# Performance work log

Hardware: AMD Instinct MI355X
Metric: run time of the kernel (lower is better)

The kernel has to match this reference:

```python
import jax, jax.numpy as jnp
import numpy as np

IN_DIM = 1024
INNER_DIM = 4096
HEADS = 16
HEAD_DIM = 64
EPS = 1e-5


def layer_norm(x, gamma, beta):
    mu = jnp.mean(x, axis=-1, keepdims=True)
    var = jnp.mean(jnp.square(x - mu), axis=-1, keepdims=True)
    return (x - mu) * jax.lax.rsqrt(var + EPS) * gamma + beta


def setup_inputs() -> dict:
    key = jax.random.key(0)
    ks = jax.random.split(key, 12)
    B, N = 2, 2048
    s_in = 1.0 / np.sqrt(IN_DIM)
    s_inner = 1.0 / np.sqrt(INNER_DIM)
    return {
        "x": jax.random.normal(ks[0], (B, N, IN_DIM), jnp.float32),
        "w_qkv": jax.random.normal(ks[1], (IN_DIM, HEADS * HEAD_DIM * 3), jnp.float32) * s_in,
        "b_qkv": jnp.zeros((HEADS * HEAD_DIM * 3,), jnp.float32),
        "w_proj": jax.random.normal(ks[2], (HEADS * HEAD_DIM, IN_DIM), jnp.float32) * s_in,
        "b_proj": jnp.zeros((IN_DIM,), jnp.float32),
        "g1": jnp.ones((IN_DIM,), jnp.float32),
        "beta1": jnp.zeros((IN_DIM,), jnp.float32),
        "w_ff1": jax.random.normal(ks[3], (IN_DIM, INNER_DIM), jnp.float32) * s_in,
        "b_ff1": jnp.zeros((INNER_DIM,), jnp.float32),
        "w_ff2": jax.random.normal(ks[4], (INNER_DIM, IN_DIM), jnp.float32) * s_inner,
        "b_ff2": jnp.zeros((IN_DIM,), jnp.float32),
        "g2": jnp.ones((IN_DIM,), jnp.float32),
        "beta2": jnp.zeros((IN_DIM,), jnp.float32),
    }


def reference(x, w_qkv, b_qkv, w_proj, b_proj, g1, beta1, w_ff1, b_ff1, w_ff2, b_ff2, g2, beta2):
    B, N, _ = x.shape
    scale = HEAD_DIM ** -0.5
    # QKV projection: (B,N,H,3D) -> (B,H,N,3D), then split as in torch chunk
    qkv = (x @ w_qkv + b_qkv).reshape(B, N, HEADS, 3 * HEAD_DIM).transpose(0, 2, 1, 3)
    q, k, v = jnp.split(qkv, 3, axis=-1)  # each (B,H,N,D)
    attn = jax.nn.softmax(jnp.einsum("bhnd,bhmd->bhnm", q, k) * scale, axis=-1)
    out = jnp.einsum("bhnm,bhmd->bhnd", attn, v).transpose(0, 2, 1, 3).reshape(B, N, HEADS * HEAD_DIM)
    out = out @ w_proj + b_proj
    # residual + LN1
    h = layer_norm(out + x, g1, beta1)
    # FFN + residual + LN2
    ff = jax.nn.relu(h @ w_ff1 + b_ff1) @ w_ff2 + b_ff2
    return layer_norm(ff + h, g2, beta2)
```

## Files before the change

kernel.cpp:

```cpp
#include <hip/hip_runtime.h>

typedef unsigned short u16;
typedef unsigned int u32;
typedef __attribute__((ext_vector_type(8))) short short8;
typedef __attribute__((ext_vector_type(4))) float float4v;

#define MB (1024 * 1024)
#define AS1 __attribute__((address_space(1)))
#define AS3 __attribute__((address_space(3)))

__device__ inline float b2f(u16 u) {
    union { u32 i; float f; } v; v.i = ((u32)u) << 16; return v.f;
}
__device__ inline u16 f2b(float f) {
    union { float f; u32 i; } v; v.f = f;
    u32 r = (v.i + 0x7FFF + ((v.i >> 16) & 1)) >> 16;
    return (u16)r;
}
__device__ inline u32 pk2(float a, float b) { return (u32)f2b(a) | ((u32)f2b(b) << 16); }
__device__ inline u32 pk2t(float a, float b) {
    return __builtin_amdgcn_perm(__float_as_uint(b), __float_as_uint(a), 0x07060302u);
}

__global__ __launch_bounds__(256) void detect_dtype(const u16* __restrict__ x, u32* __restrict__ flag) {
    __shared__ int cnt;
    if (threadIdx.x == 0) cnt = 0;
    __syncthreads();
    int hits = 0;
    for (int i = threadIdx.x; i < 512; i += 256) {
        u16 w = x[2 * i];
        int e = (w >> 7) & 0xFF;
        if (e >= 116 && e <= 134) hits++;
    }
    atomicAdd(&cnt, hits);
    __syncthreads();
    if (threadIdx.x == 0) *flag = (cnt < 256) ? 1u : 0u;
}

__global__ __launch_bounds__(256) void convert_x(const void* __restrict__ src, u16* __restrict__ dst,
                                                 int n, const u32* __restrict__ flagp) {
    int i = (blockIdx.x * 256 + threadIdx.x) * 8;
    if (i >= n) return;
    if (*flagp) {
        const float* s = (const float*)src;
        float4 f0 = *(const float4*)(s + i);
        float4 f1 = *(const float4*)(s + i + 4);
        union { uint4 v; u16 u[8]; } O;
        O.u[0] = f2b(f0.x); O.u[1] = f2b(f0.y); O.u[2] = f2b(f0.z); O.u[3] = f2b(f0.w);
        O.u[4] = f2b(f1.x); O.u[5] = f2b(f1.y); O.u[6] = f2b(f1.z); O.u[7] = f2b(f1.w);
        *(uint4*)(dst + i) = O.v;
    } else {
        *(uint4*)(dst + i) = *(const uint4*)((const u16*)src + i);
    }
}

__global__ __launch_bounds__(256) void transpose_any(const void* __restrict__ src, u16* __restrict__ dst,
                                                     int ldS, int ldD, const u32* __restrict__ flagp) {
    __shared__ alignas(16) u16 tile[64 * 78];
    int c0 = blockIdx.x * 64, r0 = blockIdx.y * 64;
    int tid = threadIdx.x;
    u32 flg = *flagp;
#pragma unroll
    for (int it = 0; it < 2; ++it) {
        int idx = tid + it * 256;
        int rr = idx >> 3, cc = idx & 7;
        union { uint4 v; u16 u[8]; } U;
        if (flg) {
            const float* s = (const float*)src + (size_t)(r0 + rr) * ldS + c0 + cc * 8;
            float4 f0 = *(const float4*)(s);
            float4 f1 = *(const float4*)(s + 4);
            U.u[0] = f2b(f0.x); U.u[1] = f2b(f0.y); U.u[2] = f2b(f0.z); U.u[3] = f2b(f0.w);
            U.u[4] = f2b(f1.x); U.u[5] = f2b(f1.y); U.u[6] = f2b(f1.z); U.u[7] = f2b(f1.w);
        } else {
            U.v = *(const uint4*)((const u16*)src + (size_t)(r0 + rr) * ldS + c0 + cc * 8);
        }
#pragma unroll
        for (int j = 0; j < 8; ++j) tile[(cc * 8 + j) * 78 + rr] = U.u[j];
    }
    __syncthreads();
#pragma unroll
    for (int it = 0; it < 2; ++it) {
        int idx = tid + it * 256;
        int rr = idx >> 3, cc = idx & 7;
        const u32* t32 = (const u32*)(tile + rr * 78);
        uint4 v;
        v.x = t32[cc * 4 + 0]; v.y = t32[cc * 4 + 1]; v.z = t32[cc * 4 + 2]; v.w = t32[cc * 4 + 3];
        *(uint4*)(dst + (size_t)(c0 + rr) * ldD + r0 + cc * 8) = v;
    }
}

__global__ __launch_bounds__(256) void v_transpose(const u16* __restrict__ qkv, u16* __restrict__ vt) {
    __shared__ alignas(16) u16 tile[64 * 78];
    int n0 = blockIdx.x * 64;
    int bh = blockIdx.y, b = bh >> 4, h = bh & 15;
    const u16* src = qkv + (size_t)b * 2048 * 3072 + h * 192 + 128;
    int tid = threadIdx.x;
#pragma unroll
    for (int it = 0; it < 2; ++it) {
        int idx = tid + it * 256;
        int rr = idx >> 3, cc = idx & 7;
        union { uint4 v; u16 u[8]; } U;
        U.v = *(const uint4*)(src + (size_t)(n0 + rr) * 3072 + cc * 8);
#pragma unroll
        for (int j = 0; j < 8; ++j) tile[(cc * 8 + j) * 78 + rr] = U.u[j];
    }
    __syncthreads();
#pragma unroll
    for (int it = 0; it < 2; ++it) {
        int idx = tid + it * 256;
        int rr = idx >> 3, cc = idx & 7;
        const u32* t32 = (const u32*)(tile + rr * 78);
        uint4 v;
        v.x = t32[cc * 4 + 0]; v.y = t32[cc * 4 + 1]; v.z = t32[cc * 4 + 2]; v.w = t32[cc * 4 + 3];
        *(uint4*)(vt + ((size_t)bh * 64 + rr) * 2048 + n0 + cc * 8) = v;
    }
}

template <int BN>
__global__ __launch_bounds__(256) void gemm_bt(const u16* __restrict__ A, const u16* __restrict__ Bt,
                                               const void* __restrict__ bias, u16* __restrict__ Cb,
                                               float* __restrict__ Cf,
                                               int M, int N, int K, int relu,
                                               const u32* __restrict__ flagp) {
    __shared__ alignas(16) u16 sA[128 * 32];
    __shared__ alignas(16) u16 sB[BN * 32];
    constexpr int WMT = (BN == 128) ? 4 : 2;
    int tid = threadIdx.x;
    int n0 = blockIdx.x * BN, m0 = blockIdx.y * 128;
    int wave = tid >> 6, lane = tid & 63, l15 = lane & 15, quad = lane >> 4;
    int wm = (BN == 128) ? (wave >> 1) * 64 : wave * 32;
    int wn = (BN == 128) ? (wave & 1) * 64 : 0;
    float4v acc[WMT][4] = {};

    for (int k0 = 0; k0 < K; k0 += 32) {
        __syncthreads();
#pragma unroll
        for (int it = 0; it < 2; ++it) {
            int idx = it * 256 + tid;
            int rr = idx >> 2, kc = idx & 3;
            __builtin_amdgcn_global_load_lds(
                (const AS1 void*)(A + (size_t)(m0 + rr) * K + k0 + kc * 8),
                (AS3 void*)&sA[(it * 256 + wave * 64) * 8], 16, 0, 0);
        }
#pragma unroll
        for (int it = 0; it < BN / 64; ++it) {
            int idx = it * 256 + tid;
            int rr = idx >> 2, kc = idx & 3;
            __builtin_amdgcn_global_load_lds(
                (const AS1 void*)(Bt + (size_t)(n0 + rr) * K + k0 + kc * 8),
                (AS3 void*)&sB[(it * 256 + wave * 64) * 8], 16, 0, 0);
        }
        __syncthreads();
        short8 a[WMT], b[4];
#pragma unroll
        for (int mi = 0; mi < WMT; ++mi) a[mi] = *(const short8*)&sA[(wm + mi * 16 + l15) * 32 + quad * 8];
#pragma unroll
        for (int ni = 0; ni < 4; ++ni) b[ni] = *(const short8*)&sB[(wn + ni * 16 + l15) * 32 + quad * 8];
#pragma unroll
        for (int mi = 0; mi < WMT; ++mi)
#pragma unroll
            for (int ni = 0; ni < 4; ++ni)
                acc[mi][ni] = __builtin_amdgcn_mfma_f32_16x16x32_bf16(a[mi], b[ni], acc[mi][ni], 0, 0, 0);
    }
    u32 flg = *flagp;
#pragma unroll
    for (int ni = 0; ni < 4; ++ni) {
        int col = n0 + wn + ni * 16 + l15;
        float bv = flg ? ((const float*)bias)[col] : b2f(((const u16*)bias)[col]);
#pragma unroll
        for (int mi = 0; mi < WMT; ++mi) {
#pragma unroll
            for (int r = 0; r < 4; ++r) {
                int row = m0 + wm + mi * 16 + quad * 4 + r;
                float v = acc[mi][ni][r] + bv;
                if (relu) v = fmaxf(v, 0.f);
                if (Cf) Cf[(size_t)row * N + col] = v;
                else    Cb[(size_t)row * N + col] = f2b(v);
            }
        }
    }
}

__global__ __launch_bounds__(256) void attn_kernel(const u16* __restrict__ qkv, const u16* __restrict__ vt,
                                                   u16* __restrict__ outp) {
    __shared__ alignas(16) u16 sK[2][64 * 64];
    __shared__ alignas(16) u16 sV[2][64 * 64];
    __shared__ alignas(16) u16 sP[4][32 * 68];
    const float C2 = 0.18033688011112042f;
    const float MT = -17.312340490667560f;
    int tid = threadIdx.x;
    int wave = tid >> 6, lane = tid & 63, l15 = lane & 15, quad = lane >> 4;
    int bh = blockIdx.x, b = bh >> 4, h = bh & 15;
    int m0 = blockIdx.y * 128 + wave * 32;
    const size_t hq = (size_t)b * 2048 * 3072 + (size_t)h * 192;
    const u16* kbase = qkv + hq + 64;
    const u16* vbase = vt + (size_t)bh * 64 * 2048;
    u16* sp = sP[wave];

    int sr = tid >> 3, sc = tid & 7;
    auto stage = [&](int buf, int n0) {
#pragma unroll
        for (int c = 0; c < 2; ++c) {
            int r = c * 32 + sr;
            __builtin_amdgcn_global_load_lds(
                (const AS1 void*)(kbase + (size_t)(n0 + r) * 3072 + ((sc ^ (r & 7)) * 8)),
                (AS3 void*)&sK[buf][c * 2048 + wave * 512], 16, 0, 0);
        }
#pragma unroll
        for (int c = 0; c < 2; ++c) {
            int r = c * 32 + sr;
            __builtin_amdgcn_global_load_lds(
                (const AS1 void*)(vbase + (size_t)r * 2048 + n0 + ((sc ^ (r & 7)) * 8)),
                (AS3 void*)&sV[buf][c * 2048 + wave * 512], 16, 0, 0);
        }
    };

    short8 qf[2][2];
#pragma unroll
    for (int mt = 0; mt < 2; ++mt)
#pragma unroll
        for (int dc = 0; dc < 2; ++dc)
            qf[mt][dc] = *(const short8*)(qkv + hq + (size_t)(m0 + mt * 16 + l15) * 3072 + dc * 32 + quad * 8);

    float4v ot[4][2] = {};
    float lacc[2] = {0.f, 0.f};

    stage(0, 0);
    for (int it = 0; it < 32; ++it) {
        int buf = it & 1;
        __syncthreads();
        if (it + 1 < 32) stage(buf ^ 1, (it + 1) * 64);

        float4v st[4][2] = {};
#pragma unroll
        for (int nt = 0; nt < 4; ++nt) {
            int row = nt * 16 + l15;
            short8 k0 = *(const short8*)&sK[buf][row * 64 + ((quad ^ (row & 7)) * 8)];
            short8 k1 = *(const short8*)&sK[buf][row * 64 + (((4 + quad) ^ (row & 7)) * 8)];
#pragma unroll
            for (int mt = 0; mt < 2; ++mt) {
                st[nt][mt] = __builtin_amdgcn_mfma_f32_16x16x32_bf16(k0, qf[mt][0], st[nt][mt], 0, 0, 0);
                st[nt][mt] = __builtin_amdgcn_mfma_f32_16x16x32_bf16(k1, qf[mt][1], st[nt][mt], 0, 0, 0);
            }
        }
#pragma unroll
        for (int mt = 0; mt < 2; ++mt) {
            float ls = 0.f;
#pragma unroll
            for (int nt = 0; nt < 4; ++nt) {
                float e0 = __builtin_amdgcn_exp2f(__builtin_fmaf(st[nt][mt][0], C2, MT));
                float e1 = __builtin_amdgcn_exp2f(__builtin_fmaf(st[nt][mt][1], C2, MT));
                float e2 = __builtin_amdgcn_exp2f(__builtin_fmaf(st[nt][mt][2], C2, MT));
                float e3 = __builtin_amdgcn_exp2f(__builtin_fmaf(st[nt][mt][3], C2, MT));
                ls += (e0 + e1) + (e2 + e3);
                *(uint2*)&sp[(mt * 16 + l15) * 68 + nt * 16 + quad * 4] =
                    make_uint2(pk2t(e0, e1), pk2t(e2, e3));
            }
            lacc[mt] += ls;
        }
        asm volatile("s_waitcnt lgkmcnt(0)" ::: "memory");
        short8 pb0[2], pb1[2];
#pragma unroll
        for (int mt = 0; mt < 2; ++mt) {
            pb0[mt] = *(const short8*)&sp[(mt * 16 + l15) * 68 + quad * 8];
            pb1[mt] = *(const short8*)&sp[(mt * 16 + l15) * 68 + 32 + quad * 8];
        }
#pragma unroll
        for (int dt = 0; dt < 4; ++dt) {
            int row = dt * 16 + l15;
            short8 v0 = *(const short8*)&sV[buf][row * 64 + ((quad ^ (row & 7)) * 8)];
            short8 v1 = *(const short8*)&sV[buf][row * 64 + (((4 + quad) ^ (row & 7)) * 8)];
#pragma unroll
            for (int mt = 0; mt < 2; ++mt) {
                ot[dt][mt] = __builtin_amdgcn_mfma_f32_16x16x32_bf16(v0, pb0[mt], ot[dt][mt], 0, 0, 0);
                ot[dt][mt] = __builtin_amdgcn_mfma_f32_16x16x32_bf16(v1, pb1[mt], ot[dt][mt], 0, 0, 0);
            }
        }
    }
#pragma unroll
    for (int mt = 0; mt < 2; ++mt) {
        float ls = lacc[mt];
        ls += __shfl_xor(ls, 16);
        ls += __shfl_xor(ls, 32);
        float inv = 1.f / ls;
        size_t row = (size_t)b * 2048 + m0 + mt * 16 + l15;
#pragma unroll
        for (int dt = 0; dt < 4; ++dt) {
            u32 lo = pk2(ot[dt][mt][0] * inv, ot[dt][mt][1] * inv);
            u32 hi = pk2(ot[dt][mt][2] * inv, ot[dt][mt][3] * inv);
            *(uint2*)(outp + row * 1024 + h * 64 + dt * 16 + quad * 4) = make_uint2(lo, hi);
        }
    }
}

__device__ inline void ld4(const void* p, int mode, u32 flg, size_t base, float* d) {
    bool isf = (mode == 2) || (mode == 1 && flg);
    if (isf) {
        float4 t = *(const float4*)((const float*)p + base);
        d[0] = t.x; d[1] = t.y; d[2] = t.z; d[3] = t.w;
    } else {
        ushort4 u = *(const ushort4*)((const u16*)p + base);
        d[0] = b2f(u.x); d[1] = b2f(u.y); d[2] = b2f(u.z); d[3] = b2f(u.w);
    }
}

__global__ __launch_bounds__(256) void ln_kernel(const void* __restrict__ in1p, int m1,
                                                 const void* __restrict__ in2p, int m2,
                                                 const void* __restrict__ g, const void* __restrict__ bt,
                                                 void* __restrict__ outp, int mout,
                                                 const u32* __restrict__ flagp) {
    __shared__ float red[8];
    u32 flg = *flagp;
    int row = blockIdx.x, tid = threadIdx.x;
    size_t base = (size_t)row * 1024 + tid * 4;
    float a[4], c[4], vv[4];
    ld4(in1p, m1, flg, base, a);
    ld4(in2p, m2, flg, base, c);
#pragma unroll
    for (int j = 0; j < 4; ++j) vv[j] = a[j] + c[j];
    float s1 = vv[0] + vv[1] + vv[2] + vv[3];
    float s2 = vv[0] * vv[0] + vv[1] * vv[1] + vv[2] * vv[2] + vv[3] * vv[3];
#pragma unroll
    for (int off = 32; off; off >>= 1) { s1 += __shfl_xor(s1, off); s2 += __shfl_xor(s2, off); }
    int wv = tid >> 6;
    if ((tid & 63) == 0) { red[wv] = s1; red[4 + wv] = s2; }
    __syncthreads();
    float S1 = red[0] + red[1] + red[2] + red[3];
    float S2 = red[4] + red[5] + red[6] + red[7];
    float mu = S1 * (1.f / 1024.f);
    float var = S2 * (1.f / 1024.f) - mu * mu;
    float rs = rsqrtf(var + 1e-5f);
    int col = tid * 4;
    float gv[4], bv[4];
    ld4(g, 1, flg, col, gv);
    ld4(bt, 1, flg, col, bv);
    bool outf = (mout == 2) || (mout == 1 && flg);
#pragma unroll
    for (int j = 0; j < 4; ++j) {
        float ov = (vv[j] - mu) * rs * gv[j] + bv[j];
        if (outf) ((float*)outp)[(size_t)row * 1024 + col + j] = ov;
        else      ((u16*)outp)[(size_t)row * 1024 + col + j] = f2b(ov);
    }
}

extern "C" void kernel_launch(void* const* d_in, const int* in_sizes, int n_in,
                              void* d_out, int out_size, void* d_ws, size_t ws_size,
                              hipStream_t stream) {
    (void)in_sizes; (void)n_in; (void)out_size; (void)ws_size;
    const void* x      = d_in[0];
    const void* w_qkv  = d_in[1];
    const void* b_qkv  = d_in[2];
    const void* w_proj = d_in[3];
    const void* b_proj = d_in[4];
    const void* g1     = d_in[5];
    const void* beta1  = d_in[6];
    const void* w_ff1  = d_in[7];
    const void* b_ff1  = d_in[8];
    const void* w_ff2  = d_in[9];
    const void* b_ff2  = d_in[10];
    const void* g2     = d_in[11];
    const void* beta2  = d_in[12];

    char* ws = (char*)d_ws;
    u16*  x_bf16 = (u16*)(ws + 0);
    u16*  wqkvT  = (u16*)(ws + 8 * MB);
    u16*  vt     = (u16*)(ws + 8 * MB);
    u16*  wprojT = (u16*)(ws + 8 * MB);
    u16*  qkv    = (u16*)(ws + 16 * MB);
    float* projo = (float*)(ws + 16 * MB);
    u16*  ff1o   = (u16*)(ws + 8 * MB);
    u16*  attno  = (u16*)(ws + 40 * MB);
    u16*  hbuf   = (u16*)(ws + 40 * MB);
    u16*  wff1T  = (u16*)(ws + 0);
    u16*  wff2T  = (u16*)(ws + 0);
    u16*  ff2o   = (u16*)(ws + 48 * MB);
    u32*  flag   = (u32*)(ws + 56 * MB);

    detect_dtype<<<1, 256, 0, stream>>>((const u16*)x, flag);
    convert_x<<<2048, 256, 0, stream>>>(x, x_bf16, 4194304, flag);
    transpose_any<<<dim3(48, 16), 256, 0, stream>>>(w_qkv, wqkvT, 3072, 1024, flag);
    gemm_bt<128><<<dim3(24, 32), 256, 0, stream>>>(x_bf16, wqkvT, b_qkv, qkv, nullptr, 4096, 3072, 1024, 0, flag);
    v_transpose<<<dim3(32, 32), 256, 0, stream>>>(qkv, vt);
    attn_kernel<<<dim3(32, 16), 256, 0, stream>>>(qkv, vt, attno);
    transpose_any<<<dim3(16, 16), 256, 0, stream>>>(w_proj, wprojT, 1024, 1024, flag);
    gemm_bt<64><<<dim3(16, 32), 256, 0, stream>>>(attno, wprojT, b_proj, nullptr, projo, 4096, 1024, 1024, 0, flag);
    ln_kernel<<<4096, 256, 0, stream>>>(projo, 2, x_bf16, 0, g1, beta1, hbuf, 0, flag);
    transpose_any<<<dim3(64, 16), 256, 0, stream>>>(w_ff1, wff1T, 4096, 1024, flag);
    gemm_bt<128><<<dim3(32, 32), 256, 0, stream>>>(hbuf, wff1T, b_ff1, ff1o, nullptr, 4096, 4096, 1024, 1, flag);
    transpose_any<<<dim3(16, 64), 256, 0, stream>>>(w_ff2, wff2T, 1024, 4096, flag);
    gemm_bt<64><<<dim3(16, 32), 256, 0, stream>>>(ff1o, wff2T, b_ff2, ff2o, nullptr, 4096, 1024, 4096, 0, flag);
    ln_kernel<<<4096, 256, 0, stream>>>(ff2o, 0, hbuf, 0, g2, beta2, d_out, 1, flag);
}
```

Before: 433.6 us.

## Split-K the narrow GEMMs and halve attention query tile for more blocks

The proj and FF2 GEMMs (N=1024, 512 blocks) now split K into two halves across blockIdx.z, each writing a partial result that the following layernorm kernel sums, so twice as many workgroups are available to fill the GPU. The attention kernel drops to 16 query rows per wave (64 per block), doubling the grid to 1024 blocks and cutting register use. The workspace buffers are remapped to hold both partials. The costs are extra partial-result traffic, bf16 rounding of the FF2 partials, and lower K/V reuse per block in attention.

Result: no change. 434.6 us (+0.2%).

```diff
diff --git a/kernel.cpp b/kernel.cpp
--- a/kernel.cpp
+++ b/kernel.cpp
@@ -116,10 +116,11 @@
     }
 }
 
-template <int BN>
+template <int BN, int KS>
 __global__ __launch_bounds__(256) void gemm_bt(const u16* __restrict__ A, const u16* __restrict__ Bt,
-                                               const void* __restrict__ bias, u16* __restrict__ Cb,
-                                               float* __restrict__ Cf,
+                                               const void* __restrict__ bias,
+                                               u16* __restrict__ Cb0, u16* __restrict__ Cb1,
+                                               float* __restrict__ Cf0, float* __restrict__ Cf1,
                                                int M, int N, int K, int relu,
                                                const u32* __restrict__ flagp) {
     __shared__ alignas(16) u16 sA[128 * 32];
@@ -127,12 +128,14 @@
     constexpr int WMT = (BN == 128) ? 4 : 2;
     int tid = threadIdx.x;
     int n0 = blockIdx.x * BN, m0 = blockIdx.y * 128;
+    int z = (KS > 1) ? blockIdx.z : 0;
+    int kz = K / KS, kbeg = z * kz;
     int wave = tid >> 6, lane = tid & 63, l15 = lane & 15, quad = lane >> 4;
     int wm = (BN == 128) ? (wave >> 1) * 64 : wave * 32;
     int wn = (BN == 128) ? (wave & 1) * 64 : 0;
     float4v acc[WMT][4] = {};
 
-    for (int k0 = 0; k0 < K; k0 += 32) {
+    for (int k0 = kbeg; k0 < kbeg + kz; k0 += 32) {
         __syncthreads();
 #pragma unroll
         for (int it = 0; it < 2; ++it) {
@@ -163,10 +166,13 @@
                 acc[mi][ni] = __builtin_amdgcn_mfma_f32_16x16x32_bf16(a[mi], b[ni], acc[mi][ni], 0, 0, 0);
     }
     u32 flg = *flagp;
+    u16* Cb = (z == 0) ? Cb0 : Cb1;
+    float* Cf = (z == 0) ? Cf0 : Cf1;
 #pragma unroll
     for (int ni = 0; ni < 4; ++ni) {
         int col = n0 + wn + ni * 16 + l15;
-        float bv = flg ? ((const float*)bias)[col] : b2f(((const u16*)bias)[col]);
+        float bv = 0.f;
+        if (z == 0) bv = flg ? ((const float*)bias)[col] : b2f(((const u16*)bias)[col]);
 #pragma unroll
         for (int mi = 0; mi < WMT; ++mi) {
 #pragma unroll
@@ -185,13 +191,13 @@
                                                    u16* __restrict__ outp) {
     __shared__ alignas(16) u16 sK[2][64 * 64];
     __shared__ alignas(16) u16 sV[2][64 * 64];
-    __shared__ alignas(16) u16 sP[4][32 * 68];
+    __shared__ alignas(16) u16 sP[4][16 * 68];
     const float C2 = 0.18033688011112042f;
     const float MT = -17.312340490667560f;
     int tid = threadIdx.x;
     int wave = tid >> 6, lane = tid & 63, l15 = lane & 15, quad = lane >> 4;
     int bh = blockIdx.x, b = bh >> 4, h = bh & 15;
-    int m0 = blockIdx.y * 128 + wave * 32;
+    int m0 = blockIdx.y * 64 + wave * 16;
     const size_t hq = (size_t)b * 2048 * 3072 + (size_t)h * 192;
     const u16* kbase = qkv + hq + 64;
     const u16* vbase = vt + (size_t)bh * 64 * 2048;
@@ -215,15 +221,13 @@
         }
     };
 
-    short8 qf[2][2];
-#pragma unroll
-    for (int mt = 0; mt < 2; ++mt)
-#pragma unroll
-        for (int dc = 0; dc < 2; ++dc)
-            qf[mt][dc] = *(const short8*)(qkv + hq + (size_t)(m0 + mt * 16 + l15) * 3072 + dc * 32 + quad * 8);
-
-    float4v ot[4][2] = {};
-    float lacc[2] = {0.f, 0.f};
+    short8 qf[2];
+#pragma unroll
+    for (int dc = 0; dc < 2; ++dc)
+        qf[dc] = *(const short8*)(qkv + hq + (size_t)(m0 + l15) * 3072 + dc * 32 + quad * 8);
+
+    float4v ot[4] = {};
+    float lacc = 0.f;
 
     stage(0, 0);
     for (int it = 0; it < 32; ++it) {
@@ -231,69 +235,53 @@
         __syncthreads();
         if (it + 1 < 32) stage(buf ^ 1, (it + 1) * 64);
 
-        float4v st[4][2] = {};
+        float4v st[4] = {};
 #pragma unroll
         for (int nt = 0; nt < 4; ++nt) {
             int row = nt * 16 + l15;
             short8 k0 = *(const short8*)&sK[buf][row * 64 + ((quad ^ (row & 7)) * 8)];
             short8 k1 = *(const short8*)&sK[buf][row * 64 + (((4 + quad) ^ (row & 7)) * 8)];
-#pragma unroll
-            for (int mt = 0; mt < 2; ++mt) {
-                st[nt][mt] = __builtin_amdgcn_mfma_f32_16x16x32_bf16(k0, qf[mt][0], st[nt][mt], 0, 0, 0);
-                st[nt][mt] = __builtin_amdgcn_mfma_f32_16x16x32_bf16(k1, qf[mt][1], st[nt][mt], 0, 0, 0);
-            }
-        }
-#pragma unroll
-        for (int mt = 0; mt < 2; ++mt) {
-            float ls = 0.f;
-#pragma unroll
-            for (int nt = 0; nt < 4; ++nt) {
-                float e0 = __builtin_amdgcn_exp2f(__builtin_fmaf(st[nt][mt][0], C2, MT));
-                float e1 = __builtin_amdgcn_exp2f(__builtin_fmaf(st[nt][mt][1], C2, MT));
-                float e2 = __builtin_amdgcn_exp2f(__builtin_fmaf(st[nt][mt][2], C2, MT));
-                float e3 = __builtin_amdgcn_exp2f(__builtin_fmaf(st[nt][mt][3], C2, MT));
-                ls += (e0 + e1) + (e2 + e3);
-                *(uint2*)&sp[(mt * 16 + l15) * 68 + nt * 16 + quad * 4] =
-                    make_uint2(pk2t(e0, e1), pk2t(e2, e3));
-            }
-            lacc[mt] += ls;
-        }
+            st[nt] = __builtin_amdgcn_mfma_f32_16x16x32_bf16(k0, qf[0], st[nt], 0, 0, 0);
+            st[nt] = __builtin_amdgcn_mfma_f32_16x16x32_bf16(k1, qf[1], st[nt], 0, 0, 0);
+        }
+        float ls = 0.f;
+#pragma unroll
+        for (int nt = 0; nt < 4; ++nt) {
+            float e0 = __builtin_amdgcn_exp2f(__builtin_fmaf(st[nt][0], C2, MT));
+            float e1 = __builtin_amdgcn_exp2f(__builtin_fmaf(st[nt][1], C2, MT));
+            float e2 = __builtin_amdgcn_exp2f(__builtin_fmaf(st[nt][2], C2, MT));
+            float e3 = __builtin_amdgcn_exp2f(__builtin_fmaf(st[nt][3], C2, MT));
+            ls += (e0 + e1) + (e2 + e3);
+            *(uint2*)&sp[l15 * 68 + nt * 16 + quad * 4] = make_uint2(pk2t(e0, e1), pk2t(e2, e3));
+        }
+        lacc += ls;
         asm volatile("s_waitcnt lgkmcnt(0)" ::: "memory");
-        short8 pb0[2], pb1[2];
-#pragma unroll
-        for (int mt = 0; mt < 2; ++mt) {
-            pb0[mt] = *(const short8*)&sp[(mt * 16 + l15) * 68 + quad * 8];
-            pb1[mt] = *(const short8*)&sp[(mt * 16 + l15) * 68 + 32 + quad * 8];
-        }
+        short8 pb0 = *(const short8*)&sp[l15 * 68 + quad * 8];
+        short8 pb1 = *(const short8*)&sp[l15 * 68 + 32 + quad * 8];
 #pragma unroll
         for (int dt = 0; dt < 4; ++dt) {
             int row = dt * 16 + l15;
             short8 v0 = *(const short8*)&sV[buf][row * 64 + ((quad ^ (row & 7)) * 8)];
             short8 v1 = *(const short8*)&sV[buf][row * 64 + (((4 + quad) ^ (row & 7)) * 8)];
-#pragma unroll
-            for (int mt = 0; mt < 2; ++mt) {
-                ot[dt][mt] = __builtin_amdgcn_mfma_f32_16x16x32_bf16(v0, pb0[mt], ot[dt][mt], 0, 0, 0);
-                ot[dt][mt] = __builtin_amdgcn_mfma_f32_16x16x32_bf16(v1, pb1[mt], ot[dt][mt], 0, 0, 0);
-            }
-        }
-    }
-#pragma unroll
-    for (int mt = 0; mt < 2; ++mt) {
-        float ls = lacc[mt];
-        ls += __shfl_xor(ls, 16);
-        ls += __shfl_xor(ls, 32);
-        float inv = 1.f / ls;
-        size_t row = (size_t)b * 2048 + m0 + mt * 16 + l15;
-#pragma unroll
-        for (int dt = 0; dt < 4; ++dt) {
-            u32 lo = pk2(ot[dt][mt][0] * inv, ot[dt][mt][1] * inv);
-            u32 hi = pk2(ot[dt][mt][2] * inv, ot[dt][mt][3] * inv);
-            *(uint2*)(outp + row * 1024 + h * 64 + dt * 16 + quad * 4) = make_uint2(lo, hi);
-        }
+            ot[dt] = __builtin_amdgcn_mfma_f32_16x16x32_bf16(v0, pb0, ot[dt], 0, 0, 0);
+            ot[dt] = __builtin_amdgcn_mfma_f32_16x16x32_bf16(v1, pb1, ot[dt], 0, 0, 0);
+        }
+    }
+    float ls = lacc;
+    ls += __shfl_xor(ls, 16);
+    ls += __shfl_xor(ls, 32);
+    float inv = 1.f / ls;
+    size_t row = (size_t)b * 2048 + m0 + l15;
+#pragma unroll
+    for (int dt = 0; dt < 4; ++dt) {
+        u32 lo = pk2(ot[dt][0] * inv, ot[dt][1] * inv);
+        u32 hi = pk2(ot[dt][2] * inv, ot[dt][3] * inv);
+        *(uint2*)(outp + row * 1024 + h * 64 + dt * 16 + quad * 4) = make_uint2(lo, hi);
     }
 }
 
 __device__ inline void ld4(const void* p, int mode, u32 flg, size_t base, float* d) {
+    if (mode < 0) { d[0] = d[1] = d[2] = d[3] = 0.f; return; }
     bool isf = (mode == 2) || (mode == 1 && flg);
     if (isf) {
         float4 t = *(const float4*)((const float*)p + base);
@@ -306,6 +294,7 @@
 
 __global__ __launch_bounds__(256) void ln_kernel(const void* __restrict__ in1p, int m1,
                                                  const void* __restrict__ in2p, int m2,
+                                                 const void* __restrict__ in3p, int m3,
                                                  const void* __restrict__ g, const void* __restrict__ bt,
                                                  void* __restrict__ outp, int mout,
                                                  const u32* __restrict__ flagp) {
@@ -313,11 +302,12 @@
     u32 flg = *flagp;
     int row = blockIdx.x, tid = threadIdx.x;
     size_t base = (size_t)row * 1024 + tid * 4;
-    float a[4], c[4], vv[4];
+    float a[4], c[4], e[4], vv[4];
     ld4(in1p, m1, flg, base, a);
     ld4(in2p, m2, flg, base, c);
-#pragma unroll
-    for (int j = 0; j < 4; ++j) vv[j] = a[j] + c[j];
+    ld4(in3p, m3, flg, base, e);
+#pragma unroll
+    for (int j = 0; j < 4; ++j) vv[j] = a[j] + c[j] + e[j];
     float s1 = vv[0] + vv[1] + vv[2] + vv[3];
     float s2 = vv[0] * vv[0] + vv[1] * vv[1] + vv[2] * vv[2] + vv[3] * vv[3];
 #pragma unroll
@@ -346,7 +336,7 @@
 extern "C" void kernel_launch(void* const* d_in, const int* in_sizes, int n_in,
                               void* d_out, int out_size, void* d_ws, size_t ws_size,
                               hipStream_t stream) {
-    (void)in_sizes; (void)n_in; (void)out_size; (void)ws_size;
+    (void)in_sizes; (void)n_in; (void)out_size;
     const void* x      = d_in[0];
     const void* w_qkv  = d_in[1];
     const void* b_qkv  = d_in[2];
@@ -364,30 +354,43 @@
     char* ws = (char*)d_ws;
     u16*  x_bf16 = (u16*)(ws + 0);
     u16*  wqkvT  = (u16*)(ws + 8 * MB);
-    u16*  vt     = (u16*)(ws + 8 * MB);
+    u16*  qkv    = (u16*)(ws + 16 * MB);
+    u16*  vt     = (u16*)(ws + 40 * MB);
+    u16*  attno  = (u16*)(ws + 48 * MB);
     u16*  wprojT = (u16*)(ws + 8 * MB);
-    u16*  qkv    = (u16*)(ws + 16 * MB);
-    float* projo = (float*)(ws + 16 * MB);
-    u16*  ff1o   = (u16*)(ws + 8 * MB);
-    u16*  attno  = (u16*)(ws + 40 * MB);
-    u16*  hbuf   = (u16*)(ws + 40 * MB);
+    float* projA = (float*)(ws + 16 * MB);
+    float* projB = (float*)(ws + 32 * MB);
+    u16*  hbuf   = (u16*)(ws + 48 * MB);
     u16*  wff1T  = (u16*)(ws + 0);
+    u16*  ff1o   = (u16*)(ws + 16 * MB);
     u16*  wff2T  = (u16*)(ws + 0);
-    u16*  ff2o   = (u16*)(ws + 48 * MB);
+    u16*  ff2A   = (u16*)(ws + 8 * MB);
+    u16*  ff2B   = (u16*)(ws + 57 * MB);
     u32*  flag   = (u32*)(ws + 56 * MB);
+    bool split_ff2 = ws_size >= (size_t)65 * MB;
 
     detect_dtype<<<1, 256, 0, stream>>>((const u16*)x, flag);
     convert_x<<<2048, 256, 0, stream>>>(x, x_bf16, 4194304, flag);
     transpose_any<<<dim3(48, 16), 256, 0, stream>>>(w_qkv, wqkvT, 3072, 1024, flag);
-    gemm_bt<128><<<dim3(24, 32), 256, 0, stream>>>(x_bf16, wqkvT, b_qkv, qkv, nullptr, 4096, 3072, 1024, 0, flag);
+    gemm_bt<128, 1><<<dim3(24, 32), 256, 0, stream>>>(x_bf16, wqkvT, b_qkv, qkv, nullptr, nullptr, nullptr,
+                                                      4096, 3072, 1024, 0, flag);
     v_transpose<<<dim3(32, 32), 256, 0, stream>>>(qkv, vt);
-    attn_kernel<<<dim3(32, 16), 256, 0, stream>>>(qkv, vt, attno);
+    attn_kernel<<<dim3(32, 32), 256, 0, stream>>>(qkv, vt, attno);
     transpose_any<<<dim3(16, 16), 256, 0, stream>>>(w_proj, wprojT, 1024, 1024, flag);
-    gemm_bt<64><<<dim3(16, 32), 256, 0, stream>>>(attno, wprojT, b_proj, nullptr, projo, 4096, 1024, 1024, 0, flag);
-    ln_kernel<<<4096, 256, 0, stream>>>(projo, 2, x_bf16, 0, g1, beta1, hbuf, 0, flag);
+    gemm_bt<64, 2><<<dim3(16, 32, 2), 256, 0, stream>>>(attno, wprojT, b_proj, nullptr, nullptr, projA, projB,
+                                                        4096, 1024, 1024, 0, flag);
+    ln_kernel<<<4096, 256, 0, stream>>>(projA, 2, projB, 2, x_bf16, 0, g1, beta1, hbuf, 0, flag);
     transpose_any<<<dim3(64, 16), 256, 0, stream>>>(w_ff1, wff1T, 4096, 1024, flag);
-    gemm_bt<128><<<dim3(32, 32), 256, 0, stream>>>(hbuf, wff1T, b_ff1, ff1o, nullptr, 4096, 4096, 1024, 1, flag);
+    gemm_bt<128, 1><<<dim3(32, 32), 256, 0, stream>>>(hbuf, wff1T, b_ff1, ff1o, nullptr, nullptr, nullptr,
+                                                      4096, 4096, 1024, 1, flag);
     transpose_any<<<dim3(16, 64), 256, 0, stream>>>(w_ff2, wff2T, 1024, 4096, flag);
-    gemm_bt<64><<<dim3(16, 32), 256, 0, stream>>>(ff1o, wff2T, b_ff2, ff2o, nullptr, 4096, 1024, 4096, 0, flag);
-    ln_kernel<<<4096, 256, 0, stream>>>(ff2o, 0, hbuf, 0, g2, beta2, d_out, 1, flag);
-}
+    if (split_ff2) {
+        gemm_bt<64, 2><<<dim3(16, 32, 2), 256, 0, stream>>>(ff1o, wff2T, b_ff2, ff2A, ff2B, nullptr, nullptr,
+                                                            4096, 1024, 4096, 0, flag);
+        ln_kernel<<<4096, 256, 0, stream>>>(ff2A, 0, ff2B, 0, hbuf, 0, g2, beta2, d_out, 1, flag);
+    } else {
+        gemm_bt<64, 1><<<dim3(16, 32), 256, 0, stream>>>(ff1o, wff2T, b_ff2, ff2A, nullptr, nullptr, nullptr,
+                                                         4096, 1024, 4096, 0, flag);
+        ln_kernel<<<4096, 256, 0, stream>>>(ff2A, 0, hbuf, 0, nullptr, -1, g2, beta2, d_out, 1, flag);
+    }
+}
```
